# Optimization experiments

Hardware: AMD Instinct MI355X
Metric: run time of the kernel (lower is better)

## Reference

```python
import jax, jax.numpy as jnp
import numpy as np

EPSILON = 1e-8
PSD_EPS = 1e-5


def _mask_norm(mask):
    # torch.norm(mask, inf, dim=1, keepdim=True): max |.| over F axis
    max_abs = jnp.max(jnp.abs(mask), axis=1, keepdims=True)
    return mask / (max_abs + EPSILON)


def _estimate_psd(mask, cm):
    # mask: [B,F,T] real; cm: [B,C,F,T] complex -> psd [B,F,C,C]
    x = jnp.transpose(cm, (0, 2, 1, 3))            # [B,F,C,T]
    m = mask[:, :, None, :]                        # [B,F,1,T]
    nom = jnp.einsum('bfct,bfdt->bfcd', x * m, jnp.conj(x))
    den = jnp.clip(jnp.sum(m, axis=-1, keepdims=True), PSD_EPS, None)
    psd = nom / den
    return psd + 1j * jnp.asarray(PSD_EPS, psd.real.dtype)


def setup_inputs() -> dict:
    key = jax.random.key(0)
    k1, k2, k3, k4 = jax.random.split(key, 4)
    B, C, F, T = 8, 8, 257, 1500
    return {
        'speech_mask': jax.random.uniform(k1, (B, F, T), dtype=jnp.float32),
        'noise_mask': jax.random.uniform(k2, (B, F, T), dtype=jnp.float32),
        'cm_real': jax.random.normal(k3, (B, C, F, T), dtype=jnp.float32),
        'cm_imag': jax.random.normal(k4, (B, C, F, T), dtype=jnp.float32),
    }


def reference(speech_mask, noise_mask, cm_real, cm_imag):
    eps = EPSILON
    cm = cm_real + 1j * cm_imag                    # [B,C,F,T] complex64
    B, C, F, T = cm.shape

    sm = _mask_norm(speech_mask)
    nm = _mask_norm(noise_mask)

    speech_psd = _estimate_psd(sm, cm) + 1j * jnp.float32(eps)   # [B,F,C,C]
    noise_psd = _estimate_psd(nm, cm) + 1j * jnp.float32(eps)

    # diagonal loading + inverse, stabilized
    eye = jnp.eye(C, dtype=noise_psd.dtype)
    noise_psd_inv = jnp.linalg.inv(noise_psd + eye * eps)
    noise_psd_inv = noise_psd_inv + 1j * jnp.float32(eps)

    A = noise_psd_inv @ speech_psd                 # [B,F,C,C]
    tr = jnp.einsum('bfcc->bf', A) + eps           # trace [B,F]

    ref_vec = jnp.zeros((B, C), dtype=A.dtype).at[:, 0].set(1.0)
    u = jnp.einsum('bfcd,bd->bfc', A, ref_vec)     # [B,F,C]
    weight = u / tr[..., None]                     # [B,F,C]
    w = jnp.transpose(weight, (0, 2, 1))           # [B,C,F]

    # apply beamformer: sum_c conj(w) * cm -> [B,F,T]
    out = jnp.einsum('bcf,bcft->bft', jnp.conj(w), cm)
    return jnp.stack([out.real, out.imag])         # [2,B,F,T] float32
```

## Files before the change

### kernel.cpp

```cpp
#include <hip/hip_runtime.h>

#define Bb 8
#define Cc 8
#define Ff 257
#define Tt 1500
#define P2 750
#define P4 375
#define BF (Bb*Ff)

__device__ __forceinline__ constexpr int utIdx(int c, int d) { return c*(17-c)/2 + (d-c); }
__device__ __forceinline__ constexpr int odIdx(int c, int d) { return 7*c - c*(c-1)/2 + (d-c-1); }

constexpr float EPSv   = 1e-8f;
constexpr float PSDEPS = 1e-5f;
constexpr float IMADD  = 1e-5f + 1e-8f;

__global__ void mask_pmax(const float* __restrict__ sm, const float* __restrict__ nm,
                          float* __restrict__ pmax_s, float* __restrict__ pmax_n) {
    int t  = blockIdx.x * 256 + threadIdx.x;
    int ch = blockIdx.y;
    int b  = blockIdx.z;
    if (t >= Tt) return;
    int f0 = ch * 33, f1 = min(Ff, f0 + 33);
    float ms = 0.f, mn = 0.f;
    for (int f = f0; f < f1; ++f) {
        ms = fmaxf(ms, fabsf(sm[(b*Ff + f)*Tt + t]));
        mn = fmaxf(mn, fabsf(nm[(b*Ff + f)*Tt + t]));
    }
    pmax_s[(b*8 + ch)*Tt + t] = ms;
    pmax_n[(b*8 + ch)*Tt + t] = mn;
}

__global__ void mask_inv(const float* __restrict__ pmax_s, const float* __restrict__ pmax_n,
                         float* __restrict__ inv_s, float* __restrict__ inv_n) {
    int t = blockIdx.x * 256 + threadIdx.x;
    int b = blockIdx.y;
    if (t >= Tt) return;
    float ms = 0.f, mn = 0.f;
    #pragma unroll
    for (int ch = 0; ch < 8; ++ch) {
        ms = fmaxf(ms, pmax_s[(b*8 + ch)*Tt + t]);
        mn = fmaxf(mn, pmax_n[(b*8 + ch)*Tt + t]);
    }
    inv_s[b*Tt + t] = 1.0f / (ms + EPSv);
    inv_n[b*Tt + t] = 1.0f / (mn + EPSv);
}

__global__ __launch_bounds__(256) __attribute__((amdgpu_waves_per_eu(4, 4)))
void mvdr_main(
    const float* __restrict__ smask, const float* __restrict__ nmask,
    const float* __restrict__ cmr,   const float* __restrict__ cmi,
    const float* __restrict__ inv_s, const float* __restrict__ inv_n,
    float* __restrict__ out)
{
    const int blk = blockIdx.x;
    const int b = blk / Ff, f = blk % Ff;
    const int tid  = threadIdx.x;
    const int wid  = tid >> 6;
    const int lane = tid & 63;
    const int msel = __builtin_amdgcn_readfirstlane(wid >> 1);
    const int part = __builtin_amdgcn_readfirstlane(wid & 1);

    const float2* sm2 = (const float2*)smask + (b*Ff + f)*P2;
    const float2* nm2 = (const float2*)nmask + (b*Ff + f)*P2;
    const float2* is2 = (const float2*)inv_s + b*P2;
    const float2* in2 = (const float2*)inv_n + b*P2;
    const float2* m2  = msel ? nm2 : sm2;
    const float2* iv2 = msel ? in2 : is2;
    const int cstride = Ff * P2;
    const float2* xr2 = (const float2*)cmr + (b*Cc)*cstride + f*P2;
    const float2* xi2 = (const float2*)cmi + (b*Cc)*cstride + f*P2;

    float acc[36];
    #pragma unroll
    for (int v = 0; v < 36; ++v) acc[v] = 0.f;
    float summ = 0.f;

    #pragma unroll 1
    for (int it = 0; it < 12; ++it) {
        int p = lane + it*64;
        const float valid = (p < P2) ? 1.0f : 0.0f;
        p = (p < P2) ? p : (P2 - 1);
        float2 mk = m2[p], iv = iv2[p];
        float2 xr[8], xi[8];
        #pragma unroll
        for (int c = 0; c < 8; ++c) { xr[c] = xr2[p + c*cstride]; xi[c] = xi2[p + c*cstride]; }
        float mx = mk.x * iv.x * valid, my = mk.y * iv.y * valid;
        if (part == 0) {
            summ += mx + my;
            #pragma unroll
            for (int c = 0; c < 8; ++c) {
                float ax = mx*xr[c].x, ay = my*xr[c].y, bx = mx*xi[c].x, by = my*xi[c].y;
                #pragma unroll
                for (int d = c; d < 8; ++d) {
                    const int k = utIdx(c, d);
                    float t0 = acc[k];
                    t0 = fmaf(ax, xr[d].x, t0); t0 = fmaf(bx, xi[d].x, t0);
                    t0 = fmaf(ay, xr[d].y, t0); t0 = fmaf(by, xi[d].y, t0);
                    acc[k] = t0;
                }
            }
        } else {
            #pragma unroll
            for (int c = 0; c < 8; ++c) {
                float ax = mx*xr[c].x, ay = my*xr[c].y, bx = mx*xi[c].x, by = my*xi[c].y;
                #pragma unroll
                for (int d = c + 1; d < 8; ++d) {
                    const int j = odIdx(c, d);
                    float t1 = acc[j];
                    t1 = fmaf(bx, xr[d].x, t1); t1 = fmaf(-ax, xi[d].x, t1);
                    t1 = fmaf(by, xr[d].y, t1); t1 = fmaf(-ay, xi[d].y, t1);
                    acc[j] = t1;
                }
            }
        }
    }

    __shared__ float Sre[36], Sim[28], Nre[36], Nim[28];
    __shared__ float sumSN[2];

    if (part == 0) {
        #pragma unroll
        for (int o = 1; o <= 32; o <<= 1) {
            summ += __shfl_xor(summ, o, 64);
            #pragma unroll
            for (int v = 0; v < 36; ++v) acc[v] += __shfl_xor(acc[v], o, 64);
        }
        if (lane == 0) {
            float* dst = msel ? Nre : Sre;
            #pragma unroll
            for (int v = 0; v < 36; ++v) dst[v] = acc[v];
            sumSN[msel] = summ;
        }
    } else {
        #pragma unroll
        for (int o = 1; o <= 32; o <<= 1) {
            #pragma unroll
            for (int v = 0; v < 28; ++v) acc[v] += __shfl_xor(acc[v], o, 64);
        }
        if (lane == 0) {
            float* dst = msel ? Nim : Sim;
            #pragma unroll
            for (int v = 0; v < 28; ++v) dst[v] = acc[v];
        }
    }
    __syncthreads();

    __shared__ float SreM[64], SimM[64];
    __shared__ float Are[128], Aim[128];
    __shared__ float dre[8], dim_[8], wre[8], wim[8];

    if (tid < 64) {
        const float den_s = fmaxf(sumSN[0], PSDEPS);
        const float den_n = fmaxf(sumSN[1], PSDEPS);
        int cc_, dd_;
        float sv, nv;
        if (tid < 36) {
            int k = tid, c = 0; while (k >= 8 - c) { k -= 8 - c; ++c; } cc_ = c; dd_ = c + k;
            sv = Sre[tid] / den_s; nv = Nre[tid] / den_n;
        } else {
            int k = tid - 36, c = 0; while (k >= 7 - c) { k -= 7 - c; ++c; } cc_ = c; dd_ = c + k + 1;
            sv = Sim[tid - 36] / den_s; nv = Nim[tid - 36] / den_n;
        }
        if (tid < 36) {
            SreM[cc_*8 + dd_] = sv; SreM[dd_*8 + cc_] = sv;
            float nvd = nv + (cc_ == dd_ ? EPSv : 0.f);
            Are[cc_*16 + dd_] = nvd; Are[dd_*16 + cc_] = nvd;
            if (cc_ == dd_) { SimM[cc_*8 + cc_] = IMADD; Aim[cc_*16 + cc_] = IMADD; }
        } else {
            SimM[cc_*8 + dd_] = IMADD + sv; SimM[dd_*8 + cc_] = IMADD - sv;
            Aim[cc_*16 + dd_] = IMADD + nv; Aim[dd_*16 + cc_] = IMADD - nv;
        }
        int r = tid >> 3, j = tid & 7;
        Are[r*16 + 8 + j] = (r == j) ? 1.f : 0.f;
        Aim[r*16 + 8 + j] = 0.f;
    }
    __syncthreads();

    {
        const bool act = tid < 64;
        const int r = (tid >> 3) & 7, cA = tid & 7;
        for (int k = 0; k < 8; ++k) {
            float pr = Are[k*16 + k], pi = Aim[k*16 + k];
            float idn = 1.0f / (pr*pr + pi*pi);
            float ipr = pr*idn, ipi = -pi*idn;
            if (act && r == k) {
                float ar0 = Are[k*16 + cA],     ai0 = Aim[k*16 + cA];
                Are[k*16 + cA]     = ar0*ipr - ai0*ipi; Aim[k*16 + cA]     = ar0*ipi + ai0*ipr;
                float ar1 = Are[k*16 + cA + 8], ai1 = Aim[k*16 + cA + 8];
                Are[k*16 + cA + 8] = ar1*ipr - ai1*ipi; Aim[k*16 + cA + 8] = ar1*ipi + ai1*ipr;
            }
            __syncthreads();
            float fr = Are[r*16 + k], fi = Aim[r*16 + k];
            float p0r = Are[k*16 + cA],     p0i = Aim[k*16 + cA];
            float p1r = Are[k*16 + cA + 8], p1i = Aim[k*16 + cA + 8];
            float o0r = 0.f, o0i = 0.f, o1r = 0.f, o1i = 0.f;
            if (r != k) {
                o0r = Are[r*16 + cA]     - (fr*p0r - fi*p0i);
                o0i = Aim[r*16 + cA]     - (fr*p0i + fi*p0r);
                o1r = Are[r*16 + cA + 8] - (fr*p1r - fi*p1i);
                o1i = Aim[r*16 + cA + 8] - (fr*p1i + fi*p1r);
            }
            __syncthreads();
            if (act && r != k) {
                Are[r*16 + cA]     = o0r; Aim[r*16 + cA]     = o0i;
                Are[r*16 + cA + 8] = o1r; Aim[r*16 + cA + 8] = o1i;
            }
            __syncthreads();
        }
    }

    if (tid < 8) {
        int c = tid;
        float ur = 0.f, ui = 0.f, tr_r = 0.f, tr_i = 0.f;
        #pragma unroll
        for (int j = 0; j < 8; ++j) {
            float vr = Are[c*16 + 8 + j], vi = Aim[c*16 + 8 + j] + EPSv;
            float s0r = SreM[j*8 + 0], s0i = SimM[j*8 + 0];
            ur += vr*s0r - vi*s0i; ui += vr*s0i + vi*s0r;
            float scr = SreM[j*8 + c], sci = SimM[j*8 + c];
            tr_r += vr*scr - vi*sci; tr_i += vr*sci + vi*scr;
        }
        dre[c] = tr_r; dim_[c] = tr_i;
        wre[c] = ur;   wim[c]  = ui;
    }
    __syncthreads();
    if (tid < 8) {
        float tr_r = EPSv, tr_i = 0.f;
        #pragma unroll
        for (int j = 0; j < 8; ++j) { tr_r += dre[j]; tr_i += dim_[j]; }
        float idn = 1.0f / (tr_r*tr_r + tr_i*tr_i);
        float ur = wre[tid], ui = wim[tid];
        wre[tid] = (ur*tr_r + ui*tr_i) * idn;
        wim[tid] = (ui*tr_r - ur*tr_i) * idn;
    }
    __syncthreads();

    float wr[8], wi[8];
    #pragma unroll
    for (int c = 0; c < 8; ++c) { wr[c] = wre[c]; wi[c] = wim[c]; }

    const int cstride4 = Ff * P4;
    const float4* xr4 = (const float4*)xr2;
    const float4* xi4 = (const float4*)xi2;
    float4* outr4 = (float4*)out + (b*Ff + f)*P4;
    float4* outi4 = (float4*)out + (Bb*Ff)*P4 + (b*Ff + f)*P4;
    for (int pp = tid; pp < P4; pp += 256) {
        float rx = 0.f, ry = 0.f, rz = 0.f, rw = 0.f;
        float ix = 0.f, iy = 0.f, iz = 0.f, iw = 0.f;
        #pragma unroll
        for (int c = 0; c < 8; ++c) {
            float4 a  = xr4[pp + c*cstride4];
            float4 bb = xi4[pp + c*cstride4];
            rx = fmaf(wr[c], a.x, fmaf(wi[c], bb.x, rx));
            ry = fmaf(wr[c], a.y, fmaf(wi[c], bb.y, ry));
            rz = fmaf(wr[c], a.z, fmaf(wi[c], bb.z, rz));
            rw = fmaf(wr[c], a.w, fmaf(wi[c], bb.w, rw));
            ix = fmaf(wr[c], bb.x, fmaf(-wi[c], a.x, ix));
            iy = fmaf(wr[c], bb.y, fmaf(-wi[c], a.y, iy));
            iz = fmaf(wr[c], bb.z, fmaf(-wi[c], a.z, iz));
            iw = fmaf(wr[c], bb.w, fmaf(-wi[c], a.w, iw));
        }
        outr4[pp] = make_float4(rx, ry, rz, rw);
        outi4[pp] = make_float4(ix, iy, iz, iw);
    }
}

extern "C" void kernel_launch(void* const* d_in, const int* in_sizes, int n_in,
                              void* d_out, int out_size, void* d_ws, size_t ws_size,
                              hipStream_t stream) {
    const float* smask = (const float*)d_in[0];
    const float* nmask = (const float*)d_in[1];
    const float* cmr   = (const float*)d_in[2];
    const float* cmi   = (const float*)d_in[3];
    float* ws = (float*)d_ws;
    float* pmax_s = ws;
    float* pmax_n = ws + 96000;
    float* inv_s  = ws + 192000;
    float* inv_n  = ws + 204000;

    mask_pmax<<<dim3(6, 8, 8), 256, 0, stream>>>(smask, nmask, pmax_s, pmax_n);
    mask_inv <<<dim3(6, 8),    256, 0, stream>>>(pmax_s, pmax_n, inv_s, inv_n);
    mvdr_main<<<BF, 256, 0, stream>>>(smask, nmask, cmr, cmi, inv_s, inv_n, (float*)d_out);
}
```

Before: 310.0 us.

## Stage PSD inputs into LDS via async global_load_lds double buffering

Replaces the direct per-lane global loads of the eight mic channels and the masks in the PSD accumulation loop with async global-to-LDS copies into two tile buffers, overlapping the next chunk's load with the current chunk's compute. Each wave loads a share of the 20 input rows and all waves read them from LDS. The diagonal terms are also split evenly between the real and imaginary waves so every wave holds 32 accumulators and runs the same shuffle reduction. This adds LDS traffic and two block barriers per iteration pair, and relies on the LDS-direct load builtin behaving as expected.

Result: slower. 373.4 us (+20.4%).

```diff
diff --git a/kernel.cpp b/kernel.cpp
--- a/kernel.cpp
+++ b/kernel.cpp
@@ -8,12 +8,16 @@
 #define P4 375
 #define BF (Bb*Ff)
 
-__device__ __forceinline__ constexpr int utIdx(int c, int d) { return c*(17-c)/2 + (d-c); }
 __device__ __forceinline__ constexpr int odIdx(int c, int d) { return 7*c - c*(c-1)/2 + (d-c-1); }
 
 constexpr float EPSv   = 1e-8f;
 constexpr float PSDEPS = 1e-5f;
 constexpr float IMADD  = 1e-5f + 1e-8f;
+
+__device__ __forceinline__ void gl2lds16(const float* g, float* l) {
+    __builtin_amdgcn_global_load_lds((const __attribute__((address_space(1))) void*)g,
+                                     (__attribute__((address_space(3))) void*)l, 16, 0, 0);
+}
 
 __global__ void mask_pmax(const float* __restrict__ sm, const float* __restrict__ nm,
                           float* __restrict__ pmax_s, float* __restrict__ pmax_n) {
@@ -61,39 +65,63 @@
     const int msel = __builtin_amdgcn_readfirstlane(wid >> 1);
     const int part = __builtin_amdgcn_readfirstlane(wid & 1);
 
-    const float2* sm2 = (const float2*)smask + (b*Ff + f)*P2;
-    const float2* nm2 = (const float2*)nmask + (b*Ff + f)*P2;
-    const float2* is2 = (const float2*)inv_s + b*P2;
-    const float2* in2 = (const float2*)inv_n + b*P2;
-    const float2* m2  = msel ? nm2 : sm2;
-    const float2* iv2 = msel ? in2 : is2;
-    const int cstride = Ff * P2;
-    const float2* xr2 = (const float2*)cmr + (b*Cc)*cstride + f*P2;
-    const float2* xi2 = (const float2*)cmi + (b*Cc)*cstride + f*P2;
-
-    float acc[36];
+    __shared__ float tile0[20*128];
+    __shared__ float tile1[20*128];
+
+    auto segbase = [&](int s) -> const float* {
+        if (s < 8)   return cmr + ((size_t)(b*Cc + s)      *Ff + f)*Tt;
+        if (s < 16)  return cmi + ((size_t)(b*Cc + (s-8))  *Ff + f)*Tt;
+        if (s == 16) return smask + ((size_t)b*Ff + f)*Tt;
+        if (s == 17) return nmask + ((size_t)b*Ff + f)*Tt;
+        if (s == 18) return inv_s + (size_t)b*Tt;
+        return inv_n + (size_t)b*Tt;
+    };
+    auto pick = [&](int j) -> const float* {
+        const float* e = segbase(2*j);
+        const float* o = segbase(2*j + 1);
+        return (lane & 32) ? o : e;
+    };
+    const float* Pa  = pick(wid);
+    const float* Pb  = pick(wid + 4);
+    const bool  has3 = (wid < 2);
+    const float* Pc  = has3 ? pick(wid + 8) : Pa;
+
+    auto stage = [&](int it, float* dst) {
+        int fi = it*128 + ((lane & 31) << 2);
+        fi = min(fi, Tt - 4);
+        gl2lds16(Pa + fi, dst + (2*wid)*128);
+        gl2lds16(Pb + fi, dst + (2*(wid+4))*128);
+        if (has3) gl2lds16(Pc + fi, dst + (2*(wid+8))*128);
+    };
+
+    float acc[32];
     #pragma unroll
-    for (int v = 0; v < 36; ++v) acc[v] = 0.f;
+    for (int v = 0; v < 32; ++v) acc[v] = 0.f;
     float summ = 0.f;
 
-    #pragma unroll 1
-    for (int it = 0; it < 12; ++it) {
-        int p = lane + it*64;
-        const float valid = (p < P2) ? 1.0f : 0.0f;
-        p = (p < P2) ? p : (P2 - 1);
-        float2 mk = m2[p], iv = iv2[p];
+    auto computeIter = [&](int it, const float* cur) {
+        const float2* c2 = (const float2*)cur;
+        float2 mk = c2[(16 + msel)*64 + lane];
+        float2 iv = c2[(18 + msel)*64 + lane];
         float2 xr[8], xi[8];
         #pragma unroll
-        for (int c = 0; c < 8; ++c) { xr[c] = xr2[p + c*cstride]; xi[c] = xi2[p + c*cstride]; }
+        for (int c = 0; c < 8; ++c) { xr[c] = c2[c*64 + lane]; xi[c] = c2[(8+c)*64 + lane]; }
+        const float valid = (lane + it*64 < P2) ? 1.0f : 0.0f;
         float mx = mk.x * iv.x * valid, my = mk.y * iv.y * valid;
         if (part == 0) {
             summ += mx + my;
             #pragma unroll
             for (int c = 0; c < 8; ++c) {
                 float ax = mx*xr[c].x, ay = my*xr[c].y, bx = mx*xi[c].x, by = my*xi[c].y;
+                if (c < 4) {
+                    float t0 = acc[28 + c];
+                    t0 = fmaf(ax, xr[c].x, t0); t0 = fmaf(bx, xi[c].x, t0);
+                    t0 = fmaf(ay, xr[c].y, t0); t0 = fmaf(by, xi[c].y, t0);
+                    acc[28 + c] = t0;
+                }
                 #pragma unroll
-                for (int d = c; d < 8; ++d) {
-                    const int k = utIdx(c, d);
+                for (int d = c + 1; d < 8; ++d) {
+                    const int k = odIdx(c, d);
                     float t0 = acc[k];
                     t0 = fmaf(ax, xr[d].x, t0); t0 = fmaf(bx, xi[d].x, t0);
                     t0 = fmaf(ay, xr[d].y, t0); t0 = fmaf(by, xi[d].y, t0);
@@ -104,6 +132,12 @@
             #pragma unroll
             for (int c = 0; c < 8; ++c) {
                 float ax = mx*xr[c].x, ay = my*xr[c].y, bx = mx*xi[c].x, by = my*xi[c].y;
+                if (c >= 4) {
+                    float t0 = acc[28 + (c - 4)];
+                    t0 = fmaf(ax, xr[c].x, t0); t0 = fmaf(bx, xi[c].x, t0);
+                    t0 = fmaf(ay, xr[c].y, t0); t0 = fmaf(by, xi[c].y, t0);
+                    acc[28 + (c - 4)] = t0;
+                }
                 #pragma unroll
                 for (int d = c + 1; d < 8; ++d) {
                     const int j = odIdx(c, d);
@@ -114,34 +148,41 @@
                 }
             }
         }
-    }
-
-    __shared__ float Sre[36], Sim[28], Nre[36], Nim[28];
+    };
+
+    stage(0, tile0);
+    __syncthreads();
+    #pragma unroll 1
+    for (int it = 0; it < 12; it += 2) {
+        stage(it + 1, tile1);
+        computeIter(it, tile0);
+        __syncthreads();
+        if (it < 10) stage(it + 2, tile0);
+        computeIter(it + 1, tile1);
+        __syncthreads();
+    }
+
+    __shared__ float OffRe[2][28], OffIm[2][28], Diagm[2][8];
     __shared__ float sumSN[2];
 
-    if (part == 0) {
-        #pragma unroll
-        for (int o = 1; o <= 32; o <<= 1) {
-            summ += __shfl_xor(summ, o, 64);
-            #pragma unroll
-            for (int v = 0; v < 36; ++v) acc[v] += __shfl_xor(acc[v], o, 64);
-        }
-        if (lane == 0) {
-            float* dst = msel ? Nre : Sre;
-            #pragma unroll
-            for (int v = 0; v < 36; ++v) dst[v] = acc[v];
+    #pragma unroll
+    for (int o = 1; o <= 32; o <<= 1) {
+        if (part == 0) summ += __shfl_xor(summ, o, 64);
+        #pragma unroll
+        for (int v = 0; v < 32; ++v) acc[v] += __shfl_xor(acc[v], o, 64);
+    }
+    if (lane == 0) {
+        if (part == 0) {
+            #pragma unroll
+            for (int v = 0; v < 28; ++v) OffRe[msel][v] = acc[v];
+            #pragma unroll
+            for (int v = 0; v < 4; ++v) Diagm[msel][v] = acc[28 + v];
             sumSN[msel] = summ;
-        }
-    } else {
-        #pragma unroll
-        for (int o = 1; o <= 32; o <<= 1) {
-            #pragma unroll
-            for (int v = 0; v < 28; ++v) acc[v] += __shfl_xor(acc[v], o, 64);
-        }
-        if (lane == 0) {
-            float* dst = msel ? Nim : Sim;
-            #pragma unroll
-            for (int v = 0; v < 28; ++v) dst[v] = acc[v];
+        } else {
+            #pragma unroll
+            for (int v = 0; v < 28; ++v) OffIm[msel][v] = acc[v];
+            #pragma unroll
+            for (int v = 0; v < 4; ++v) Diagm[msel][4 + v] = acc[28 + v];
         }
     }
     __syncthreads();
@@ -157,10 +198,11 @@
         float sv, nv;
         if (tid < 36) {
             int k = tid, c = 0; while (k >= 8 - c) { k -= 8 - c; ++c; } cc_ = c; dd_ = c + k;
-            sv = Sre[tid] / den_s; nv = Nre[tid] / den_n;
+            if (cc_ == dd_) { sv = Diagm[0][cc_] / den_s; nv = Diagm[1][cc_] / den_n; }
+            else { int o = odIdx(cc_, dd_); sv = OffRe[0][o] / den_s; nv = OffRe[1][o] / den_n; }
         } else {
             int k = tid - 36, c = 0; while (k >= 7 - c) { k -= 7 - c; ++c; } cc_ = c; dd_ = c + k + 1;
-            sv = Sim[tid - 36] / den_s; nv = Nim[tid - 36] / den_n;
+            sv = OffIm[0][tid - 36] / den_s; nv = OffIm[1][tid - 36] / den_n;
         }
         if (tid < 36) {
             SreM[cc_*8 + dd_] = sv; SreM[dd_*8 + cc_] = sv;
@@ -241,8 +283,8 @@
     for (int c = 0; c < 8; ++c) { wr[c] = wre[c]; wi[c] = wim[c]; }
 
     const int cstride4 = Ff * P4;
-    const float4* xr4 = (const float4*)xr2;
-    const float4* xi4 = (const float4*)xi2;
+    const float4* xr4 = (const float4*)(cmr + ((size_t)(b*Cc)*Ff + f)*Tt);
+    const float4* xi4 = (const float4*)(cmi + ((size_t)(b*Cc)*Ff + f)*Tt);
     float4* outr4 = (float4*)out + (b*Ff + f)*P4;
     float4* outi4 = (float4*)out + (Bb*Ff)*P4 + (b*Ff + f)*P4;
     for (int pp = tid; pp < P4; pp += 256) {
```
